# Optimization experiments

Measured on AMD Instinct MI355X. Metric: run time of the kernel, lower is better.

The kernel has to match this reference:

```python
import jax, jax.numpy as jnp
import numpy as np

S = 100                     # MC weight samples
B = 128                     # batch
CONV1 = (100, 20, 1, 5, 5)  # (S, Cout, Cin, kh, kw)
CONV2 = (100, 50, 20, 5, 5)
AFF1 = (100, 500, 800)      # (S, out, in)
AFF2 = (100, 10, 500)
W_OFF = np.cumsum([0, 500, 25000, 400000, 5000])
B_OFF = np.cumsum([0, 20, 50, 500, 10])
NW, NB = 430500, 580


def _softplus(r):
    return jnp.log1p(jnp.exp(r))  # sigma_T(rho) = log(1 + exp(rho))


def _conv(h, w, b):
    # h: (B, S or 1, Cin, H, W); w: (S, Cout, Cin, kh, kw); b: (S, Cout)
    def one(xs, ws):  # xs: (B,Cin,H,W), ws: (Cout,Cin,kh,kw)
        return jax.lax.conv_general_dilated(xs, ws, (1, 1), 'VALID')
    if h.shape[1] == 1:  # shared input broadcast over samples (first layer)
        out = jax.vmap(one, in_axes=(None, 0), out_axes=1)(h[:, 0], w)
    else:
        out = jax.vmap(one, in_axes=(1, 0), out_axes=1)(h, w)
    return out + b[None, :, :, None, None]  # (B,S,Cout,H',W')


def _maxpool(h):  # 2x2 stride-2 over trailing spatial dims
    return jax.lax.reduce_window(h, -jnp.inf, jax.lax.max,
                                 (1, 1, 1, 2, 2), (1, 1, 1, 2, 2), 'VALID')


def setup_inputs() -> dict:
    key = jax.random.key(0)
    ks = jax.random.split(key, 4)
    x = jax.random.normal(ks[0], (B, 1, 28, 28), dtype=jnp.float32)
    e = jax.random.normal(ks[1], (S, NW + NB), dtype=jnp.float32)
    mu_w = jax.random.normal(ks[2], (NW,), dtype=jnp.float32) * 0.05
    rho_w = jnp.ones((NW,), dtype=jnp.float32) * 0.5
    mu_b = jax.random.normal(ks[3], (NB,), dtype=jnp.float32) * 0.05
    rho_b = jnp.ones((NB,), dtype=jnp.float32) * 0.5
    return {"x": x, "e": e, "mu_w": mu_w, "rho_w": rho_w,
            "mu_b": mu_b, "rho_b": rho_b}


def reference(x, e, mu_w, rho_w, mu_b, rho_b):
    # reparameterized per-sample weights: (S, NW) and (S, NB)
    w = mu_w + _softplus(rho_w) * e[:, :NW]
    b = mu_b + _softplus(rho_b) * e[:, NW:]

    h = x[:, None]  # (B,1,1,28,28): singleton MC dim broadcasts
    # conv1 + relu + pool
    h = _conv(h, w[:, W_OFF[0]:W_OFF[1]].reshape(CONV1), b[:, B_OFF[0]:B_OFF[1]])
    h = _maxpool(jax.nn.relu(h))                     # (B,S,20,12,12)
    # conv2 + relu + pool
    h = _conv(h, w[:, W_OFF[1]:W_OFF[2]].reshape(CONV2), b[:, B_OFF[1]:B_OFF[2]])
    h = _maxpool(jax.nn.relu(h))                     # (B,S,50,4,4)
    h = h.reshape(h.shape[0], h.shape[1], -1)        # (B,S,800)
    # aff1 + relu
    w3 = w[:, W_OFF[2]:W_OFF[3]].reshape(AFF1)
    h = jax.nn.relu(jnp.einsum('bsi,soi->bso', h, w3) + b[None, :, B_OFF[2]:B_OFF[3]])
    # aff2 + log_softmax
    w4 = w[:, W_OFF[3]:W_OFF[4]].reshape(AFF2)
    h = jnp.einsum('bsi,soi->bso', h, w4) + b[None, :, B_OFF[3]:B_OFF[4]]
    h = jax.nn.log_softmax(h, axis=-1)               # (B,S,10)
    return h.mean(axis=1)                            # eval path: mean over MC samples
```

## Files before the change

kernel.cpp:

```cpp
#include <hip/hip_runtime.h>
#include <math.h>

#define Sn 100
#define Bn 128
#define NWc 430500
#define EWc 431080

typedef __attribute__((ext_vector_type(8)))  short bhalf8;
typedef __attribute__((ext_vector_type(16))) float fx16;

__device__ __forceinline__ float sp_f(float r){
    return fmaxf(r, 0.f) + log1pf(__expf(-fabsf(r)));
}
__device__ __forceinline__ ushort bfr(float f){
    union { float f; uint u; } c; c.f = f;
    uint r = (c.u + 0x7FFFu + ((c.u >> 16) & 1u)) >> 16;
    return (ushort)r;
}

__global__ void k00_sp(const float* __restrict__ rho_w, const float* __restrict__ rho_b,
                       float* __restrict__ sp_all){
    int i = blockIdx.x * blockDim.x + threadIdx.x;
    if (i < NWc)      sp_all[i] = sp_f(rho_w[i]);
    else if (i < EWc) sp_all[i] = sp_f(rho_b[i - NWc]);
}

__global__ __launch_bounds__(256) void k0_w3t(const float* __restrict__ e,
        const float* __restrict__ mu_w, const float* __restrict__ sp_all,
        ushort* __restrict__ w3){
    __shared__ __align__(16) ushort ls[2][20*808];
    int oc = blockIdx.x;
    int sp = blockIdx.y;
    int s0 = sp * 2;
    int o0 = oc * 20;
    int tid = threadIdx.x;
    const float* e0 = e + (size_t)s0*EWc + 25500 + (size_t)o0*800;
    const float* e1 = e0 + EWc;
    const float* mb = mu_w   + 25500 + (size_t)o0*800;
    const float* pb = sp_all + 25500 + (size_t)o0*800;
    #pragma unroll 2
    for (int j = tid; j < 4000; j += 256){
        int o = j / 200, k4 = j - o*200;
        float4 mv = *(const float4*)(mb + j*4);
        float4 sv = *(const float4*)(pb + j*4);
        float4 ev0 = *(const float4*)(e0 + j*4);
        float4 ev1 = *(const float4*)(e1 + j*4);
        ushort4 t0, t1;
        t0.x = bfr(fmaf(sv.x, ev0.x, mv.x));
        t0.y = bfr(fmaf(sv.y, ev0.y, mv.y));
        t0.z = bfr(fmaf(sv.z, ev0.z, mv.z));
        t0.w = bfr(fmaf(sv.w, ev0.w, mv.w));
        t1.x = bfr(fmaf(sv.x, ev1.x, mv.x));
        t1.y = bfr(fmaf(sv.y, ev1.y, mv.y));
        t1.z = bfr(fmaf(sv.z, ev1.z, mv.z));
        t1.w = bfr(fmaf(sv.w, ev1.w, mv.w));
        *(ushort4*)&ls[0][o*808 + k4*4] = t0;
        *(ushort4*)&ls[1][o*808 + k4*4] = t1;
    }
    __syncthreads();
    if (tid < 200){
        int kt = tid >> 3, l8 = tid & 7;
        #pragma unroll
        for (int ss = 0; ss < 2; ++ss){
            ushort* wb = w3 + (size_t)(s0 + ss)*400000 + kt*16000 + o0*32;
            #pragma unroll
            for (int it = 0; it < 10; ++it){
                int idx = it*8 + l8;
                int o = idx >> 2, kp = (idx & 3)*8;
                uint4 v = *(const uint4*)&ls[ss][o*808 + kt*32 + kp];
                *(uint4*)(wb + idx*8) = v;
            }
        }
    }
}

__global__ void k0_small(const float* __restrict__ e, const float* __restrict__ mu_w,
                       const float* __restrict__ sp_all, const float* __restrict__ mu_b,
                       float* __restrict__ w1, ushort* __restrict__ w2r,
                       float* __restrict__ w4, float* __restrict__ ball){
    const int per = 31080;
    int idx = blockIdx.x * blockDim.x + threadIdx.x;
    if (idx >= Sn * per) return;
    int s = idx / per, j = idx % per;
    if (j < 500){
        float v = fmaf(sp_all[j], e[(size_t)s*EWc + j], mu_w[j]);
        w1[s*500 + j] = v;
    } else if (j < 25500){
        int g = j;
        float v = fmaf(sp_all[g], e[(size_t)s*EWc + g], mu_w[g]);
        int j2 = j - 500;
        int oc = j2 / 500, rem = j2 % 500;
        int ic = rem / 25, kk = rem % 25;
        w2r[(size_t)s*51200 + (kk*64 + oc)*32 + ic] = bfr(v);
    } else if (j < 30500){
        int g = 425500 + (j - 25500);
        float v = fmaf(sp_all[g], e[(size_t)s*EWc + g], mu_w[g]);
        w4[s*5000 + (j - 25500)] = v;
    } else {
        int k = j - 30500;
        float v = fmaf(sp_all[NWc + k], e[(size_t)s*EWc + NWc + k], mu_b[k]);
        ball[s*580 + k] = v;
    }
}

__global__ __launch_bounds__(256, 2) void k1_conv1(const float* __restrict__ x,
        const float* __restrict__ w1, const float* __restrict__ ball,
        ushort* __restrict__ h1p){
    __shared__ __align__(16) float xs[784];
    __shared__ __align__(16) float w1s[500];
    __shared__ float b1s[20];
    __shared__ __align__(16) ushort ots[2880];
    int bid = blockIdx.x;
    int s = bid / Bn, b = bid % Bn;
    int tid = threadIdx.x;
    for (int i = tid; i < 784; i += 256) xs[i] = x[b*784 + i];
    for (int i = tid; i < 500; i += 256) w1s[i] = w1[s*500 + i];
    if (tid < 20) b1s[tid] = ball[s*580 + tid];
    __syncthreads();
    if (tid < 240){
        int c = tid / 12, y = tid % 12;

        float acc0[24], acc1[24];
        #pragma unroll
        for (int i = 0; i < 24; ++i){ acc0[i] = 0.f; acc1[i] = 0.f; }

        #pragma unroll
        for (int ky = 0; ky < 5; ++ky){
            float rlo[28], rhi[28];
            const float* plo = &xs[(2*y + ky) * 28];
            const float* phi = &xs[(2*y + ky + 1) * 28];
            #pragma unroll
            for (int cc = 0; cc < 28; cc += 4){
                float4 v0 = *(const float4*)(plo + cc);
                rlo[cc] = v0.x; rlo[cc+1] = v0.y; rlo[cc+2] = v0.z; rlo[cc+3] = v0.w;
                float4 v1 = *(const float4*)(phi + cc);
                rhi[cc] = v1.x; rhi[cc+1] = v1.y; rhi[cc+2] = v1.z; rhi[cc+3] = v1.w;
            }
            #pragma unroll
            for (int kx = 0; kx < 5; ++kx){
                float wv = w1s[c*25 + ky*5 + kx];
                #pragma unroll
                for (int cx = 0; cx < 24; ++cx){
                    acc0[cx] = fmaf(rlo[cx + kx], wv, acc0[cx]);
                    acc1[cx] = fmaf(rhi[cx + kx], wv, acc1[cx]);
                }
            }
        }
        float bias = b1s[c];
        #pragma unroll
        for (int px = 0; px < 12; ++px){
            float m = fmaxf(fmaxf(acc0[2*px], acc0[2*px+1]),
                            fmaxf(acc1[2*px], acc1[2*px+1]));
            ots[(y*12 + px)*20 + c] = bfr(fmaxf(m + bias, 0.f));
        }
    }
    __syncthreads();
    const uint* o32 = (const uint*)ots;
    uint* g32 = (uint*)(h1p + (s*Bn + b)*2880);
    for (int j = tid; j < 1440; j += 256) g32[j] = o32[j];
}

__global__ __launch_bounds__(256, 4) void k2_direct(const ushort* __restrict__ h1p,
        const ushort* __restrict__ w2r, const float* __restrict__ ball,
        ushort* __restrict__ h2p){
    __shared__ __align__(16) ushort img[4*4608];
    __shared__ __align__(16) ushort Bls[2048];
    int bid = blockIdx.x;
    int s = bid >> 5, g = bid & 31;
    int tid = threadIdx.x;
    const uint* g32 = (const uint*)(h1p + (size_t)(s*Bn + g*4)*2880);
    uint* l32 = (uint*)img;
    for (int j = tid; j < 5760; j += 256){
        int im = j / 1440, r = j - im*1440;
        int p = r / 10, u = r - p*10;
        l32[im*2304 + ((p*16 + u) ^ ((p & 7) << 2))] = g32[j];
    }
    for (int j = tid; j < 3456; j += 256){
        int im = j / 864, r = j - im*864;
        int p = r / 6, u = 10 + (r - p*6);
        l32[im*2304 + ((p*16 + u) ^ ((p & 7) << 2))] = 0u;
    }

    int oc_w = tid >> 2, c_w = tid & 3;
    int P = ((c_w >> 1)*2 + (oc_w >> 5))*64 + (c_w & 1)*32 + (oc_w & 31);
    uint4* bdst = (uint4*)&Bls[P*8];
    const uint4* bsrc = (const uint4*)(w2r + (size_t)(s*25)*2048) + tid;
    uint4 breg = bsrc[0];

    int wv = tid >> 6, l = tid & 63;
    int l31 = l & 31, q = l >> 5;
    const ushort* imgw = img + wv*4608;
    int pixb0 = ((l31      ) >> 3)*12 + (l31 & 7);
    int pixb1 = ((l31 + 32 ) >> 3)*12 + (l31 & 7);
    int lam = q*32 + l31;
    fx16 acc00 = (fx16)0.f, acc01 = (fx16)0.f, acc10 = (fx16)0.f, acc11 = (fx16)0.f;

    *bdst = breg;
    __syncthreads();

    #pragma unroll 1
    for (int kk = 0; kk < 25; ++kk){
        if (kk < 24) breg = bsrc[(kk + 1)*256];

        int ky = kk / 5, kx = kk - ky*5;
        int poff = ky*12 + kx;
        int p0 = pixb0 + poff, p1 = pixb1 + poff;
        int sw0 = (p0 & 7) << 3, sw1 = (p1 & 7) << 3;

        bhalf8 a00 = *(const bhalf8*)(imgw + ((p0*32 +      q*8) ^ sw0));
        bhalf8 a10 = *(const bhalf8*)(imgw + ((p1*32 +      q*8) ^ sw1));
        bhalf8 a01 = *(const bhalf8*)(imgw + ((p0*32 + 16 + q*8) ^ sw0));
        bhalf8 a11 = *(const bhalf8*)(imgw + ((p1*32 + 16 + q*8) ^ sw1));
        bhalf8 b0  = *(const bhalf8*)&Bls[       lam*8];
        bhalf8 b1  = *(const bhalf8*)&Bls[ 512 + lam*8];
        bhalf8 b2  = *(const bhalf8*)&Bls[1024 + lam*8];
        bhalf8 b3  = *(const bhalf8*)&Bls[1536 + lam*8];

        acc00 = __builtin_amdgcn_mfma_f32_32x32x16_bf16(a00, b0, acc00, 0, 0, 0);
        acc01 = __builtin_amdgcn_mfma_f32_32x32x16_bf16(a00, b1, acc01, 0, 0, 0);
        acc10 = __builtin_amdgcn_mfma_f32_32x32x16_bf16(a10, b0, acc10, 0, 0, 0);
        acc11 = __builtin_amdgcn_mfma_f32_32x32x16_bf16(a10, b1, acc11, 0, 0, 0);
        acc00 = __builtin_amdgcn_mfma_f32_32x32x16_bf16(a01, b2, acc00, 0, 0, 0);
        acc01 = __builtin_amdgcn_mfma_f32_32x32x16_bf16(a01, b3, acc01, 0, 0, 0);
        acc10 = __builtin_amdgcn_mfma_f32_32x32x16_bf16(a11, b2, acc10, 0, 0, 0);
        acc11 = __builtin_amdgcn_mfma_f32_32x32x16_bf16(a11, b3, acc11, 0, 0, 0);

        if (kk < 24){
            __syncthreads();
            *bdst = breg;
            __syncthreads();
        }
    }
    int b = g*4 + wv;
    ushort* dst = h2p + (size_t)s*102400 + (size_t)b*32;
    #pragma unroll
    for (int nt = 0; nt < 2; ++nt){
        int oc = nt*32 + l31;
        if (oc >= 50) continue;
        float bias = ball[s*580 + 20 + oc];
        #pragma unroll
        for (int mt = 0; mt < 2; ++mt){
            fx16 a;
            if (nt == 0) a = mt ? acc10 : acc00;
            else         a = mt ? acc11 : acc01;
            #pragma unroll
            for (int gp = 0; gp < 2; ++gp){
                float p0 = fmaxf(fmaxf(a[8*gp+0], a[8*gp+1]), fmaxf(a[8*gp+4], a[8*gp+5]));
                float p1 = fmaxf(fmaxf(a[8*gp+2], a[8*gp+3]), fmaxf(a[8*gp+6], a[8*gp+7]));
                p0 = fmaxf(p0 + bias, 0.f);
                p1 = fmaxf(p1 + bias, 0.f);
                int py = mt*2 + gp;
                int i  = oc*16 + py*4 + 2*q;
                uint pk = (uint)bfr(p0) | ((uint)bfr(p1) << 16);
                *(uint*)(dst + (i >> 5)*4096 + (i & 31)) = pk;
            }
        }
    }
}

#define ICS 40
__global__ __launch_bounds__(256) void k3_mfma(const ushort* __restrict__ h2p,
        const ushort* __restrict__ w3, const float* __restrict__ ball,
        float* __restrict__ h3){
    __shared__ __align__(16) ushort As[128*ICS];
    __shared__ __align__(16) ushort Bsh[64*ICS];
    int bid = blockIdx.x;
    int s = bid >> 3, nblk = bid & 7;
    int o0 = nblk * 64;
    int tid = threadIdx.x;
    int wv = tid >> 6, l = tid & 63, l31 = l & 31, q = l >> 5;
    int wm = wv >> 1, wn = wv & 1;
    fx16 acc0 = (fx16)0.f, acc1 = (fx16)0.f;
    int rr = tid >> 2, rk = (tid & 3)*8;
    const ushort* Abase = h2p + (size_t)s*102400;
    const ushort* Bbase = w3  + (size_t)s*400000 + (size_t)o0*32;
    bool bvalid = (o0 + rr) < 500;
    const uint4 z4 = make_uint4(0u,0u,0u,0u);

    uint4 ar0, ar1, br;
    ar0 = *(const uint4*)(Abase + rr*32 + rk);
    ar1 = *(const uint4*)(Abase + (rr + 64)*32 + rk);
    br  = bvalid ? *(const uint4*)(Bbase + rr*32 + rk) : z4;

    for (int kt = 0; kt < 25; ++kt){
        __syncthreads();
        *(uint4*)&As[rr*ICS + rk]        = ar0;
        *(uint4*)&As[(rr + 64)*ICS + rk] = ar1;
        *(uint4*)&Bsh[rr*ICS + rk]       = br;
        __syncthreads();
        if (kt < 24){
            ar0 = *(const uint4*)(Abase + (kt+1)*4096 + rr*32 + rk);
            ar1 = *(const uint4*)(Abase + (kt+1)*4096 + (rr + 64)*32 + rk);
            br  = bvalid ? *(const uint4*)(Bbase + (kt+1)*16000 + rr*32 + rk) : z4;
        }
        #pragma unroll
        for (int ks = 0; ks < 2; ++ks){
            bhalf8 a0 = *(const bhalf8*)&As[(wm*64      + l31)*ICS + ks*16 + q*8];
            bhalf8 a1 = *(const bhalf8*)&As[(wm*64 + 32 + l31)*ICS + ks*16 + q*8];
            bhalf8 bb = *(const bhalf8*)&Bsh[(wn*32 + l31)*ICS + ks*16 + q*8];
            acc0 = __builtin_amdgcn_mfma_f32_32x32x16_bf16(a0, bb, acc0, 0, 0, 0);
            acc1 = __builtin_amdgcn_mfma_f32_32x32x16_bf16(a1, bb, acc1, 0, 0, 0);
        }
    }
    int o = o0 + wn*32 + l31;
    if (o < 500){
        float bias = ball[s*580 + 70 + o];
        #pragma unroll
        for (int mt = 0; mt < 2; ++mt){
            fx16 a = mt ? acc1 : acc0;
            #pragma unroll
            for (int reg = 0; reg < 16; ++reg){
                int row = (reg & 3) + 8*(reg >> 2) + 4*q;
                int b = wm*64 + mt*32 + row;
                h3[(size_t)(s*Bn + b)*500 + o] = fmaxf(a[reg] + bias, 0.f);
            }
        }
    }
}

__global__ __launch_bounds__(256) void k4a(const float* __restrict__ h3,
        const float* __restrict__ w4, const float* __restrict__ ball,
        float* __restrict__ lsw){
    int wv = threadIdx.x >> 6, lane = threadIdx.x & 63;
    int p = blockIdx.x*4 + wv;
    int s = p / Bn;
    const float* hp = &h3[(size_t)p*500];
    const float* wp = &w4[(size_t)s*5000];
    float part[10];
    #pragma unroll
    for (int o = 0; o < 10; ++o) part[o] = 0.f;
    for (int i = lane; i < 500; i += 64){
        float hv = hp[i];
        #pragma unroll
        for (int o = 0; o < 10; ++o)
            part[o] = fmaf(hv, wp[o*500 + i], part[o]);
    }
    #pragma unroll
    for (int o = 0; o < 10; ++o){
        #pragma unroll
        for (int d = 1; d < 64; d <<= 1)
            part[o] += __shfl_xor(part[o], d);
    }
    float v[10]; float m = -INFINITY;
    #pragma unroll
    for (int o = 0; o < 10; ++o){
        v[o] = part[o] + ball[s*580 + 570 + o];
        m = fmaxf(m, v[o]);
    }
    float sum = 0.f;
    #pragma unroll
    for (int o = 0; o < 10; ++o) sum += __expf(v[o] - m);
    float lse = m + __logf(sum);
    if (lane == 0){
        #pragma unroll
        for (int o = 0; o < 10; ++o) lsw[p*10 + o] = v[o] - lse;
    }
}

__global__ void k4b(const float* __restrict__ lsw, float* __restrict__ outp){
    int j = blockIdx.x * blockDim.x + threadIdx.x;
    if (j >= Bn*10) return;
    int b = j / 10, o = j % 10;
    float acc = 0.f;
    for (int s2 = 0; s2 < Sn; ++s2) acc += lsw[(s2*Bn + b)*10 + o];
    outp[j] = acc * (1.f / (float)Sn);
}

extern "C" void kernel_launch(void* const* d_in, const int* in_sizes, int n_in,
                              void* d_out, int out_size, void* d_ws, size_t ws_size,
                              hipStream_t stream){
    const float* x     = (const float*)d_in[0];
    const float* e     = (const float*)d_in[1];
    const float* mu_w  = (const float*)d_in[2];
    const float* rho_w = (const float*)d_in[3];
    const float* mu_b  = (const float*)d_in[4];
    const float* rho_b = (const float*)d_in[5];
    float* ws   = (float*)d_ws;
    float* w1     = ws;
    float* w4     = w1 + 50000;
    float* ball   = w4 + 500000;
    float* h3     = ball + 58000;
    float* lsw    = h3 + 6400000;
    float* sp_all = lsw + 128000;
    ushort* h1p = (ushort*)(sp_all + 431080);
    ushort* h2p = h1p + 36864000;
    ushort* w2r = h2p + 10240000;
    ushort* w3  = w2r + 5120000;
    float* outp = (float*)d_out;

    hipMemsetAsync(w2r, 0, (size_t)Sn*51200*2, stream);
    k00_sp   <<<(EWc + 255)/256, 256, 0, stream>>>(rho_w, rho_b, sp_all);
    k0_w3t   <<<dim3(25, 50), 256, 0, stream>>>(e, mu_w, sp_all, w3);
    k0_small <<<(Sn*31080 + 255)/256, 256, 0, stream>>>(e, mu_w, sp_all, mu_b, w1, w2r, w4, ball);
    k1_conv1 <<<Sn*Bn, 256, 0, stream>>>(x, w1, ball, h1p);
    k2_direct<<<Sn*32, 256, 0, stream>>>(h1p, w2r, ball, h2p);
    k3_mfma  <<<Sn*8, 256, 0, stream>>>(h2p, w3, ball, h3);
    k4a      <<<3200, 256, 0, stream>>>(h3, w4, ball, lsw);
    k4b      <<<(Bn*10 + 255)/256, 256, 0, stream>>>(lsw, outp);
}
```

Before: 526.8 us.

## Double-buffer conv2 weight tiles and compact the unswizzled image layout in LDS

The conv2 MFMA kernel now keeps two LDS buffers for the per-tap weight tile, so each iteration writes the next tile into the idle buffer and needs one barrier per tap instead of two. The per-image LDS layout drops the 32-channel padded, XOR-swizzled rows for compact 24-element rows. The zero padding for channels 20-23 is kept and lanes with q=1 feed zeros into the second K-half, which shrinks LDS use and may allow more resident blocks. The risk is LDS bank conflicts on the now-unswizzled A reads, and a lane-divergent select around the second pair of A loads.

Result: no change. 525.8 us (-0.2%).

```diff
diff --git a/kernel.cpp b/kernel.cpp
--- a/kernel.cpp
+++ b/kernel.cpp
@@ -163,8 +163,8 @@
 __global__ __launch_bounds__(256, 4) void k2_direct(const ushort* __restrict__ h1p,
         const ushort* __restrict__ w2r, const float* __restrict__ ball,
         ushort* __restrict__ h2p){
-    __shared__ __align__(16) ushort img[4*4608];
-    __shared__ __align__(16) ushort Bls[2048];
+    __shared__ __align__(16) ushort img[4*3456];
+    __shared__ __align__(16) ushort Bls[2][2048];
     int bid = blockIdx.x;
     int s = bid >> 5, g = bid & 31;
     int tid = threadIdx.x;
@@ -173,61 +173,64 @@
     for (int j = tid; j < 5760; j += 256){
         int im = j / 1440, r = j - im*1440;
         int p = r / 10, u = r - p*10;
-        l32[im*2304 + ((p*16 + u) ^ ((p & 7) << 2))] = g32[j];
-    }
-    for (int j = tid; j < 3456; j += 256){
-        int im = j / 864, r = j - im*864;
-        int p = r / 6, u = 10 + (r - p*6);
-        l32[im*2304 + ((p*16 + u) ^ ((p & 7) << 2))] = 0u;
+        l32[im*1728 + p*12 + u] = g32[j];
+    }
+    for (int j = tid; j < 1152; j += 256){
+        int im = j / 288, r = j - im*288;
+        int p = r >> 1, u = 10 + (r & 1);
+        l32[im*1728 + p*12 + u] = 0u;
     }
 
     int oc_w = tid >> 2, c_w = tid & 3;
     int P = ((c_w >> 1)*2 + (oc_w >> 5))*64 + (c_w & 1)*32 + (oc_w & 31);
-    uint4* bdst = (uint4*)&Bls[P*8];
+    uint4* bd0 = (uint4*)&Bls[0][P*8];
+    uint4* bd1 = (uint4*)&Bls[1][P*8];
     const uint4* bsrc = (const uint4*)(w2r + (size_t)(s*25)*2048) + tid;
     uint4 breg = bsrc[0];
+    *bd0 = breg;
 
     int wv = tid >> 6, l = tid & 63;
     int l31 = l & 31, q = l >> 5;
-    const ushort* imgw = img + wv*4608;
+    const ushort* imgw = img + wv*3456;
     int pixb0 = ((l31      ) >> 3)*12 + (l31 & 7);
     int pixb1 = ((l31 + 32 ) >> 3)*12 + (l31 & 7);
     int lam = q*32 + l31;
     fx16 acc00 = (fx16)0.f, acc01 = (fx16)0.f, acc10 = (fx16)0.f, acc11 = (fx16)0.f;
-
-    *bdst = breg;
+    const bhalf8 zero8 = (bhalf8)(short)0;
+
     __syncthreads();
 
     #pragma unroll 1
     for (int kk = 0; kk < 25; ++kk){
+        int cur = kk & 1;
         if (kk < 24) breg = bsrc[(kk + 1)*256];
 
         int ky = kk / 5, kx = kk - ky*5;
         int poff = ky*12 + kx;
-        int p0 = pixb0 + poff, p1 = pixb1 + poff;
-        int sw0 = (p0 & 7) << 3, sw1 = (p1 & 7) << 3;
-
-        bhalf8 a00 = *(const bhalf8*)(imgw + ((p0*32 +      q*8) ^ sw0));
-        bhalf8 a10 = *(const bhalf8*)(imgw + ((p1*32 +      q*8) ^ sw1));
-        bhalf8 a01 = *(const bhalf8*)(imgw + ((p0*32 + 16 + q*8) ^ sw0));
-        bhalf8 a11 = *(const bhalf8*)(imgw + ((p1*32 + 16 + q*8) ^ sw1));
-        bhalf8 b0  = *(const bhalf8*)&Bls[       lam*8];
-        bhalf8 b1  = *(const bhalf8*)&Bls[ 512 + lam*8];
-        bhalf8 b2  = *(const bhalf8*)&Bls[1024 + lam*8];
-        bhalf8 b3  = *(const bhalf8*)&Bls[1536 + lam*8];
-
+        const ushort* r0 = imgw + (pixb0 + poff)*24;
+        const ushort* r1 = imgw + (pixb1 + poff)*24;
+        const ushort* Bc = Bls[cur];
+
+        bhalf8 a00 = *(const bhalf8*)(r0 + q*8);
+        bhalf8 a10 = *(const bhalf8*)(r1 + q*8);
+        bhalf8 b0  = *(const bhalf8*)&Bc[       lam*8];
+        bhalf8 b1  = *(const bhalf8*)&Bc[ 512 + lam*8];
         acc00 = __builtin_amdgcn_mfma_f32_32x32x16_bf16(a00, b0, acc00, 0, 0, 0);
         acc01 = __builtin_amdgcn_mfma_f32_32x32x16_bf16(a00, b1, acc01, 0, 0, 0);
         acc10 = __builtin_amdgcn_mfma_f32_32x32x16_bf16(a10, b0, acc10, 0, 0, 0);
         acc11 = __builtin_amdgcn_mfma_f32_32x32x16_bf16(a10, b1, acc11, 0, 0, 0);
+
+        bhalf8 a01 = (q == 0) ? *(const bhalf8*)(r0 + 16) : zero8;
+        bhalf8 a11 = (q == 0) ? *(const bhalf8*)(r1 + 16) : zero8;
+        bhalf8 b2  = *(const bhalf8*)&Bc[1024 + lam*8];
+        bhalf8 b3  = *(const bhalf8*)&Bc[1536 + lam*8];
         acc00 = __builtin_amdgcn_mfma_f32_32x32x16_bf16(a01, b2, acc00, 0, 0, 0);
         acc01 = __builtin_amdgcn_mfma_f32_32x32x16_bf16(a01, b3, acc01, 0, 0, 0);
         acc10 = __builtin_amdgcn_mfma_f32_32x32x16_bf16(a11, b2, acc10, 0, 0, 0);
         acc11 = __builtin_amdgcn_mfma_f32_32x32x16_bf16(a11, b3, acc11, 0, 0, 0);
 
         if (kk < 24){
-            __syncthreads();
-            *bdst = breg;
+            *(cur ? bd0 : bd1) = breg;
             __syncthreads();
         }
     }
```
